# Kernel optimization log

Hardware: AMD Instinct MI355X
Metric: run time of the kernel (lower is better)

## Reference

```python
import jax, jax.numpy as jnp
import numpy as np

NO = 16          # config['Max_Object']
NT = 8           # config['Max_Time']
FEAT = 512       # config['feat_dims']
VIS_IN = 2048
TGT = 24


def setup_inputs() -> dict:
    key = jax.random.key(0)
    ks = jax.random.split(key, 10)
    b = 16
    N = NT * 2 * NO  # 256
    s = lambda k, *sh: jax.random.normal(k, sh, dtype=jnp.float32) * 0.02
    return {
        "src": jax.random.normal(ks[0], (b, 1, 1, N, VIS_IN), dtype=jnp.float32),
        "tgt_rel": jax.random.randint(ks[1], (b * NT * NO * NO,), 0, TGT, dtype=jnp.int64),
        "w1": s(ks[2], VIS_IN, FEAT), "b1": jnp.zeros((FEAT,), jnp.float32),
        "w2": s(ks[3], FEAT, FEAT),   "b2": jnp.zeros((FEAT,), jnp.float32),
        "wf": s(ks[4], FEAT, FEAT),   "bf": jnp.zeros((FEAT,), jnp.float32),
        "wr": s(ks[5], 2 * FEAT, TGT), "br": jnp.zeros((TGT,), jnp.float32),
    }


def reference(src, tgt_rel, w1, b1, w2, b2, wf, bf, wr, br):
    b = src.shape[0]
    BT = b * NT
    # src[:, 0, 0, :, :] -> (b, N, D) -> (b*NT, 2*NO, D); take visual part [:2048]
    x = src[:, 0, 0, :, :].reshape(BT, 2 * NO, -1)[:, :, :VIS_IN]
    # fc_vis: MLP 2048 -> FEAT -> FEAT
    h = jnp.maximum(x @ w1 + b1, 0.0) @ w2 + b2          # (BT, 2NO, FEAT)
    node_feats = h @ wf + bf                             # fc_fusion
    # vectorized replacement of the NOxNO python double loop:
    # edge[:, i*NO + (j-NO), :] = cat(node[:, i], node[:, j])  for i<NO<=j
    subj = jnp.broadcast_to(node_feats[:, :NO, None, :], (BT, NO, NO, FEAT))
    obj = jnp.broadcast_to(node_feats[:, None, NO:, :], (BT, NO, NO, FEAT))
    edge_feats = jnp.concatenate([subj, obj], axis=-1).reshape(BT, NO * NO, 2 * FEAT)
    out = (edge_feats @ wr + br).reshape(-1, TGT)        # fc_rel
    tgt = tgt_rel.reshape(-1)
    w_cls = jnp.asarray([1.0] + [100.0] * (TGT - 1), dtype=out.dtype)
    logp = jax.nn.log_softmax(out, axis=-1)
    nll = -jnp.take_along_axis(logp, tgt[:, None], axis=1)[:, 0]
    ww = w_cls[tgt]
    loss = jnp.sum(ww * nll) / jnp.sum(ww)  # torch weighted cross_entropy (mean)
    return out, tgt, loss
```

## Files before the change

### kernel.cpp

```cpp
#include <hip/hip_runtime.h>
#include <cstddef>
#include <cstdint>

#define NOBJ   16
#define FEAT   512
#define VIS    2048
#define NTGT   24
#define MROWS  4096
#define EROWS  32768

typedef __attribute__((ext_vector_type(8))) short short8;
typedef __attribute__((ext_vector_type(4))) float f32x4;

__device__ __forceinline__ float bf2f(unsigned short u) {
    union { unsigned int i; float f; } v; v.i = ((unsigned int)u) << 16; return v.f;
}
__device__ __forceinline__ unsigned short f2bf(float f) {
    union { float f; unsigned int i; } v; v.f = f;
    const unsigned int x = v.i;
    return (unsigned short)((x + 0x7fffu + ((x >> 16) & 1u)) >> 16);
}
__device__ __forceinline__ short8 pack8(const float4 a, const float4 b) {
    short8 r;
    r[0] = (short)f2bf(a.x); r[1] = (short)f2bf(a.y);
    r[2] = (short)f2bf(a.z); r[3] = (short)f2bf(a.w);
    r[4] = (short)f2bf(b.x); r[5] = (short)f2bf(b.y);
    r[6] = (short)f2bf(b.z); r[7] = (short)f2bf(b.w);
    return r;
}

__global__ void zero_kernel(float* __restrict__ p, int n) {
    const int i = blockIdx.x * 256 + threadIdx.x;
    if (i < n) p[i] = 0.f;
}

__global__ __launch_bounds__(256)
void wtrans(const float* __restrict__ w1, unsigned short* __restrict__ w1t) {
    __shared__ float tile[32][33];
    const int k0 = blockIdx.x * 32;
    const int n0 = blockIdx.y * 32;
    const int tx = threadIdx.x & 31, ty = threadIdx.x >> 5;
    #pragma unroll
    for (int r = 0; r < 32; r += 8)
        tile[ty + r][tx] = w1[(size_t)(k0 + ty + r) * FEAT + n0 + tx];
    __syncthreads();
    #pragma unroll
    for (int r = 0; r < 32; r += 8)
        w1t[(size_t)(n0 + ty + r) * VIS + k0 + tx] = f2bf(tile[tx][ty + r]);
}

__global__ __launch_bounds__(256)
void wchain1(const float* __restrict__ wf, const float* __restrict__ bfv,
             const float* __restrict__ wr, float* __restrict__ t1) {
    const int c    = threadIdx.x;
    const int krow = blockIdx.x * 8 + threadIdx.y;
    const int h    = blockIdx.z;
    const int j0   = blockIdx.y * 128;
    if (krow > 512) return;
    const float* rowp = (krow < 512) ? (wf + (size_t)krow * FEAT) : bfv;
    const int ce = (c < NTGT) ? c : NTGT - 1;
    const float* wrp = wr + ((size_t)h * FEAT + j0) * NTGT + ce;
    float s = 0.f;
    #pragma unroll 8
    for (int j = 0; j < 128; ++j)
        s = fmaf(rowp[j0 + j], wrp[(size_t)j * NTGT], s);
    if (c < NTGT) atomicAdd(&t1[((size_t)h * 513 + krow) * 32 + c], s);
}

__global__ __launch_bounds__(256)
void wchain2(const float* __restrict__ w2, const float* __restrict__ b2,
             const float* __restrict__ t1, float* __restrict__ wAB) {
    const int c  = threadIdx.x;
    const int r  = blockIdx.x * 8 + threadIdx.y;
    const int h  = blockIdx.z;
    const int k0 = blockIdx.y * 128;
    if (r > 512) return;
    const float* rowp = (r < 512) ? (w2 + (size_t)r * FEAT) : b2;
    const int ce = (c < NTGT) ? c : NTGT - 1;
    const float* tp = t1 + ((size_t)h * 513 + k0) * 32 + ce;
    float s = 0.f;
    #pragma unroll 8
    for (int k = 0; k < 128; ++k)
        s = fmaf(rowp[k0 + k], tp[(size_t)k * 32], s);
    if (r == 512 && blockIdx.y == 0)
        s += t1[((size_t)h * 513 + 512) * 32 + ce];
    if (c < NTGT) atomicAdd(&wAB[((size_t)h * 513 + r) * 32 + c], s);
}

__global__ __launch_bounds__(256)
void gemm1(const float* __restrict__ src, const unsigned short* __restrict__ w1t,
           const float* __restrict__ b1, unsigned short* __restrict__ h) {
    __shared__ __align__(16) unsigned short As[2][128 * 64];
    __shared__ __align__(16) unsigned short Bs[2][64 * 64];

    const int bid = blockIdx.x;
    const int xcd = bid & 7;
    const int k8  = bid >> 3;
    const int xb  = k8 & 7;
    const int yb  = (xcd << 2) | (k8 >> 3);
    const int m0 = yb * 128;
    const int n0 = xb * 64;

    const int tid  = threadIdx.x;
    const int lane = tid & 63;
    const int wid  = tid >> 6;
    const int wr = wid >> 1, wc = wid & 1;

    f32x4  acc[4][2] = {};
    float4 areg[4][2];
    short8 breg[2];

    #pragma unroll
    for (int q = 0; q < 4; ++q) {
        const int s = q * 256 + tid, row = s >> 3, c = s & 7, cd = c ^ (row & 7);
        const float* gp = src + (size_t)(m0 + row) * VIS + (cd << 3);
        areg[q][0] = *reinterpret_cast<const float4*>(gp);
        areg[q][1] = *reinterpret_cast<const float4*>(gp + 4);
    }
    #pragma unroll
    for (int q = 0; q < 2; ++q) {
        const int s = q * 256 + tid, n = s >> 3, c = s & 7, cd = c ^ (n & 7);
        breg[q] = *reinterpret_cast<const short8*>(w1t + (size_t)(n0 + n) * VIS + (cd << 3));
    }
    #pragma unroll
    for (int q = 0; q < 4; ++q) {
        const int s = q * 256 + tid, row = s >> 3, c = s & 7;
        *reinterpret_cast<short8*>(&As[0][(row << 6) + (c << 3)]) = pack8(areg[q][0], areg[q][1]);
    }
    #pragma unroll
    for (int q = 0; q < 2; ++q) {
        const int s = q * 256 + tid, n = s >> 3, c = s & 7;
        *reinterpret_cast<short8*>(&Bs[0][(n << 6) + (c << 3)]) = breg[q];
    }
    __syncthreads();

    int cur = 0;
    for (int t = 0; t < VIS / 64; ++t) {
        const int kn = (t + 1) * 64;
        if (t + 1 < VIS / 64) {
            #pragma unroll
            for (int q = 0; q < 4; ++q) {
                const int s = q * 256 + tid, row = s >> 3, c = s & 7, cd = c ^ (row & 7);
                const float* gp = src + (size_t)(m0 + row) * VIS + kn + (cd << 3);
                areg[q][0] = *reinterpret_cast<const float4*>(gp);
                areg[q][1] = *reinterpret_cast<const float4*>(gp + 4);
            }
            #pragma unroll
            for (int q = 0; q < 2; ++q) {
                const int s = q * 256 + tid, n = s >> 3, c = s & 7, cd = c ^ (n & 7);
                breg[q] = *reinterpret_cast<const short8*>(w1t + (size_t)(n0 + n) * VIS + kn + (cd << 3));
            }
        }
        #pragma unroll
        for (int k2 = 0; k2 < 2; ++k2) {
            short8 af[4], bfr[2];
            #pragma unroll
            for (int fr = 0; fr < 4; ++fr) {
                const int row = wr * 64 + fr * 16 + (lane & 15);
                const int cw  = ((k2 << 2) + (lane >> 4)) ^ (row & 7);
                af[fr] = *reinterpret_cast<const short8*>(&As[cur][(row << 6) + (cw << 3)]);
            }
            #pragma unroll
            for (int fc = 0; fc < 2; ++fc) {
                const int n  = wc * 32 + fc * 16 + (lane & 15);
                const int cw = ((k2 << 2) + (lane >> 4)) ^ (n & 7);
                bfr[fc] = *reinterpret_cast<const short8*>(&Bs[cur][(n << 6) + (cw << 3)]);
            }
            #pragma unroll
            for (int fr = 0; fr < 4; ++fr)
                #pragma unroll
                for (int fc = 0; fc < 2; ++fc)
                    acc[fr][fc] = __builtin_amdgcn_mfma_f32_16x16x32_bf16(
                        af[fr], bfr[fc], acc[fr][fc], 0, 0, 0);
        }
        if (t + 1 < VIS / 64) {
            const int nxt = cur ^ 1;
            #pragma unroll
            for (int q = 0; q < 4; ++q) {
                const int s = q * 256 + tid, row = s >> 3, c = s & 7;
                *reinterpret_cast<short8*>(&As[nxt][(row << 6) + (c << 3)]) =
                    pack8(areg[q][0], areg[q][1]);
            }
            #pragma unroll
            for (int q = 0; q < 2; ++q) {
                const int s = q * 256 + tid, n = s >> 3, c = s & 7;
                *reinterpret_cast<short8*>(&Bs[nxt][(n << 6) + (c << 3)]) = breg[q];
            }
        }
        __syncthreads();
        cur ^= 1;
    }

    #pragma unroll
    for (int fc = 0; fc < 2; ++fc) {
        const int n = n0 + wc * 32 + fc * 16 + (lane & 15);
        const float bias = b1[n];
        #pragma unroll
        for (int fr = 0; fr < 4; ++fr) {
            const int mb = m0 + wr * 64 + fr * 16 + ((lane >> 4) << 2);
            #pragma unroll
            for (int r = 0; r < 4; ++r) {
                const float v = fmaxf(acc[fr][fc][r] + bias, 0.f);
                h[(size_t)(mb + r) * FEAT + n] = f2bf(v);
            }
        }
    }
}

__global__ __launch_bounds__(192)
void proj(const unsigned short* __restrict__ h, const float* __restrict__ wAB,
          float* __restrict__ Ap, float* __restrict__ Bp) {
    __shared__ float rows[8][FEAT];
    const int g0 = blockIdx.x * 8;
    const int hh = (g0 >> 4) & 1;
    const int tid = threadIdx.x;
    for (int s = tid; s < 512; s += 192) {
        const int row = s >> 6, c8 = (s & 63) << 3;
        short8 v = *reinterpret_cast<const short8*>(h + (size_t)(g0 + row) * FEAT + c8);
        #pragma unroll
        for (int e = 0; e < 8; ++e)
            rows[row][c8 + e] = bf2f((unsigned short)v[e]);
    }
    __syncthreads();
    const int c = tid % NTGT, rr = tid / NTGT;
    const float* wp = wAB + (size_t)hh * 513 * 32 + c;
    float s = 0.f;
    #pragma unroll 8
    for (int k = 0; k < FEAT; ++k)
        s = fmaf(rows[rr][k], wp[(size_t)k * 32], s);
    s += wp[(size_t)512 * 32];
    const int g = g0 + rr, bt = g >> 5, i = g & 15;
    float* dst = (g & 16) ? Bp : Ap;
    dst[((size_t)bt * NOBJ + i) * NTGT + c] = s;
}

__global__ __launch_bounds__(256)
void out_loss_kernel(const float* __restrict__ Ap, const float* __restrict__ Bp,
                     const float* __restrict__ br, const int* __restrict__ tgt,
                     float* __restrict__ out, float* __restrict__ out_tgt,
                     float* __restrict__ acc) {
    const int r   = blockIdx.x * 256 + threadIdx.x;
    const int bt  = r >> 8;
    const int rem = r & 255;
    const int i   = rem >> 4;
    const int j   = rem & 15;
    const float4* ap4 = reinterpret_cast<const float4*>(Ap + ((size_t)bt * NOBJ + i) * NTGT);
    const float4* bp4 = reinterpret_cast<const float4*>(Bp + ((size_t)bt * NOBJ + j) * NTGT);
    const int tg = tgt[r];

    float vals[NTGT];
    float mx = -1e30f, vtg = 0.f;
    #pragma unroll
    for (int q = 0; q < 6; ++q) {
        const float4 a = ap4[q], b = bp4[q];
        vals[q * 4 + 0] = a.x + b.x + br[q * 4 + 0];
        vals[q * 4 + 1] = a.y + b.y + br[q * 4 + 1];
        vals[q * 4 + 2] = a.z + b.z + br[q * 4 + 2];
        vals[q * 4 + 3] = a.w + b.w + br[q * 4 + 3];
    }
    #pragma unroll
    for (int t = 0; t < NTGT; ++t) {
        mx = fmaxf(mx, vals[t]);
        if (t == tg) vtg = vals[t];
    }
    float se = 0.f;
    #pragma unroll
    for (int t = 0; t < NTGT; ++t) se += expf(vals[t] - mx);
    const float lse = mx + logf(se);

    float4* o4 = reinterpret_cast<float4*>(out + (size_t)r * NTGT);
    #pragma unroll
    for (int q = 0; q < 6; ++q)
        o4[q] = make_float4(vals[q * 4], vals[q * 4 + 1], vals[q * 4 + 2], vals[q * 4 + 3]);
    out_tgt[r] = (float)tg;

    const float wcl = (tg == 0) ? 1.f : 100.f;
    float p1 = wcl * (lse - vtg);
    float p2 = wcl;
    #pragma unroll
    for (int off = 32; off > 0; off >>= 1) {
        p1 += __shfl_down(p1, off);
        p2 += __shfl_down(p2, off);
    }
    __shared__ float s1[4], s2[4];
    const int lane = threadIdx.x & 63;
    const int wid  = threadIdx.x >> 6;
    if (lane == 0) { s1[wid] = p1; s2[wid] = p2; }
    __syncthreads();
    if (threadIdx.x == 0) {
        atomicAdd(&acc[0], s1[0] + s1[1] + s1[2] + s1[3]);
        atomicAdd(&acc[1], s2[0] + s2[1] + s2[2] + s2[3]);
    }
}

__global__ void final_loss(const float* __restrict__ acc, float* __restrict__ loss) {
    loss[0] = acc[0] / acc[1];
}

extern "C" void kernel_launch(void* const* d_in, const int* in_sizes, int n_in,
                              void* d_out, int out_size, void* d_ws, size_t ws_size,
                              hipStream_t stream) {
    const float* src = (const float*)d_in[0];
    const int*   tgt = (const int*)d_in[1];
    const float* w1  = (const float*)d_in[2];
    const float* b1  = (const float*)d_in[3];
    const float* w2  = (const float*)d_in[4];
    const float* b2  = (const float*)d_in[5];
    const float* wf  = (const float*)d_in[6];
    const float* bfv = (const float*)d_in[7];
    const float* wr  = (const float*)d_in[8];
    const float* br  = (const float*)d_in[9];

    float* ws = (float*)d_ws;
    unsigned short* w1t = (unsigned short*)(ws);
    unsigned short* h   = (unsigned short*)(ws + 524288);
    float* t1  = ws + 1572864;
    float* wAB = ws + 1605696;
    float* acc = ws + 1638528;
    float* Ap  = ws + 1638532;
    float* Bp  = ws + 1687684;

    float* out_logits = (float*)d_out;
    float* out_tgt    = out_logits + (size_t)EROWS * NTGT;
    float* out_lossp  = out_tgt + EROWS;

    zero_kernel<<<257, 256, 0, stream>>>(t1, 65666);
    wtrans<<<dim3(64, 16), 256, 0, stream>>>(w1, w1t);
    wchain1<<<dim3(65, 4, 2), dim3(32, 8), 0, stream>>>(wf, bfv, wr, t1);
    wchain2<<<dim3(65, 4, 2), dim3(32, 8), 0, stream>>>(w2, b2, t1, wAB);
    gemm1<<<256, 256, 0, stream>>>(src, w1t, b1, h);
    proj<<<512, 192, 0, stream>>>(h, wAB, Ap, Bp);
    out_loss_kernel<<<EROWS / 256, 256, 0, stream>>>(Ap, Bp, br, tgt,
                                                     out_logits, out_tgt, acc);
    final_loss<<<1, 1, 0, stream>>>(acc, out_lossp);
}
```

Baseline: 172.3 us.

## Restructure weight chain, projection, gemm tiling and loss reduction pipeline

```diff
diff --git a/kernel.cpp b/kernel.cpp
--- a/kernel.cpp
+++ b/kernel.cpp
@@ -12,9 +12,6 @@
 typedef __attribute__((ext_vector_type(8))) short short8;
 typedef __attribute__((ext_vector_type(4))) float f32x4;
 
-__device__ __forceinline__ float bf2f(unsigned short u) {
-    union { unsigned int i; float f; } v; v.i = ((unsigned int)u) << 16; return v.f;
-}
 __device__ __forceinline__ unsigned short f2bf(float f) {
     union { float f; unsigned int i; } v; v.f = f;
     const unsigned int x = v.i;
@@ -29,11 +26,6 @@
     return r;
 }
 
-__global__ void zero_kernel(float* __restrict__ p, int n) {
-    const int i = blockIdx.x * 256 + threadIdx.x;
-    if (i < n) p[i] = 0.f;
-}
-
 __global__ __launch_bounds__(256)
 void wtrans(const float* __restrict__ w1, unsigned short* __restrict__ w1t) {
     __shared__ float tile[32][33];
@@ -52,63 +44,72 @@
 __global__ __launch_bounds__(256)
 void wchain1(const float* __restrict__ wf, const float* __restrict__ bfv,
              const float* __restrict__ wr, float* __restrict__ t1) {
+    __shared__ float wrs[FEAT * NTGT];
+    const int h = blockIdx.y;
+    const float* wrh = wr + (size_t)h * FEAT * NTGT;
+    for (int idx = threadIdx.y * 32 + threadIdx.x; idx < FEAT * NTGT; idx += 256)
+        wrs[idx] = wrh[idx];
+    __syncthreads();
     const int c    = threadIdx.x;
     const int krow = blockIdx.x * 8 + threadIdx.y;
-    const int h    = blockIdx.z;
-    const int j0   = blockIdx.y * 128;
     if (krow > 512) return;
     const float* rowp = (krow < 512) ? (wf + (size_t)krow * FEAT) : bfv;
     const int ce = (c < NTGT) ? c : NTGT - 1;
-    const float* wrp = wr + ((size_t)h * FEAT + j0) * NTGT + ce;
     float s = 0.f;
     #pragma unroll 8
-    for (int j = 0; j < 128; ++j)
-        s = fmaf(rowp[j0 + j], wrp[(size_t)j * NTGT], s);
-    if (c < NTGT) atomicAdd(&t1[((size_t)h * 513 + krow) * 32 + c], s);
+    for (int j = 0; j < FEAT; ++j)
+        s = fmaf(rowp[j], wrs[j * NTGT + ce], s);
+    if (c < NTGT) t1[((size_t)h * 513 + krow) * 32 + c] = s;
 }
 
 __global__ __launch_bounds__(256)
 void wchain2(const float* __restrict__ w2, const float* __restrict__ b2,
-             const float* __restrict__ t1, float* __restrict__ wAB) {
-    const int c  = threadIdx.x;
-    const int r  = blockIdx.x * 8 + threadIdx.y;
-    const int h  = blockIdx.z;
-    const int k0 = blockIdx.y * 128;
+             const float* __restrict__ t1, unsigned short* __restrict__ wABt,
+             float* __restrict__ biasAB) {
+    __shared__ float t1s[FEAT * NTGT];
+    const int h = blockIdx.y;
+    for (int idx = threadIdx.y * 32 + threadIdx.x; idx < FEAT * NTGT; idx += 256) {
+        const int row = idx / NTGT, col = idx - row * NTGT;
+        t1s[idx] = t1[((size_t)h * 513 + row) * 32 + col];
+    }
+    __syncthreads();
+    const int c = threadIdx.x;
+    const int r = blockIdx.x * 8 + threadIdx.y;
     if (r > 512) return;
     const float* rowp = (r < 512) ? (w2 + (size_t)r * FEAT) : b2;
     const int ce = (c < NTGT) ? c : NTGT - 1;
-    const float* tp = t1 + ((size_t)h * 513 + k0) * 32 + ce;
     float s = 0.f;
     #pragma unroll 8
-    for (int k = 0; k < 128; ++k)
-        s = fmaf(rowp[k0 + k], tp[(size_t)k * 32], s);
-    if (r == 512 && blockIdx.y == 0)
-        s += t1[((size_t)h * 513 + 512) * 32 + ce];
-    if (c < NTGT) atomicAdd(&wAB[((size_t)h * 513 + r) * 32 + c], s);
+    for (int k = 0; k < FEAT; ++k)
+        s = fmaf(rowp[k], t1s[k * NTGT + ce], s);
+    if (c < NTGT) {
+        const int q = h * NTGT + c;
+        if (r < 512) wABt[(size_t)q * FEAT + r] = f2bf(s);
+        else         biasAB[q] = s + t1[((size_t)h * 513 + 512) * 32 + c];
+    }
 }
 
 __global__ __launch_bounds__(256)
 void gemm1(const float* __restrict__ src, const unsigned short* __restrict__ w1t,
            const float* __restrict__ b1, unsigned short* __restrict__ h) {
     __shared__ __align__(16) unsigned short As[2][128 * 64];
-    __shared__ __align__(16) unsigned short Bs[2][64 * 64];
+    __shared__ __align__(16) unsigned short Bs[2][32 * 64];
 
     const int bid = blockIdx.x;
     const int xcd = bid & 7;
     const int k8  = bid >> 3;
-    const int xb  = k8 & 7;
-    const int yb  = (xcd << 2) | (k8 >> 3);
+    const int xb  = k8 & 15;
+    const int yb  = (xcd << 2) | (k8 >> 4);
     const int m0 = yb * 128;
-    const int n0 = xb * 64;
+    const int n0 = xb * 32;
 
     const int tid  = threadIdx.x;
     const int lane = tid & 63;
     const int wid  = tid >> 6;
-    const int wr = wid >> 1, wc = wid & 1;
-
-    f32x4  acc[4][2] = {};
+
+    f32x4  acc[2][2] = {};
     float4 areg[4][2];
-    short8 breg[2];
+    short8 breg;
 
     #pragma unroll
     for (int q = 0; q < 4; ++q) {
@@ -117,20 +118,18 @@
         areg[q][0] = *reinterpret_cast<const float4*>(gp);
         areg[q][1] = *reinterpret_cast<const float4*>(gp + 4);
     }
-    #pragma unroll
-    for (int q = 0; q < 2; ++q) {
-        const int s = q * 256 + tid, n = s >> 3, c = s & 7, cd = c ^ (n & 7);
-        breg[q] = *reinterpret_cast<const short8*>(w1t + (size_t)(n0 + n) * VIS + (cd << 3));
+    {
+        const int n = tid >> 3, c = tid & 7, cd = c ^ (n & 7);
+        breg = *reinterpret_cast<const short8*>(w1t + (size_t)(n0 + n) * VIS + (cd << 3));
     }
     #pragma unroll
     for (int q = 0; q < 4; ++q) {
         const int s = q * 256 + tid, row = s >> 3, c = s & 7;
         *reinterpret_cast<short8*>(&As[0][(row << 6) + (c << 3)]) = pack8(areg[q][0], areg[q][1]);
     }
-    #pragma unroll
-    for (int q = 0; q < 2; ++q) {
-        const int s = q * 256 + tid, n = s >> 3, c = s & 7;
-        *reinterpret_cast<short8*>(&Bs[0][(n << 6) + (c << 3)]) = breg[q];
+    {
+        const int n = tid >> 3, c = tid & 7;
+        *reinterpret_cast<short8*>(&Bs[0][(n << 6) + (c << 3)]) = breg;
     }
     __syncthreads();
 
@@ -145,29 +144,26 @@
                 areg[q][0] = *reinterpret_cast<const float4*>(gp);
                 areg[q][1] = *reinterpret_cast<const float4*>(gp + 4);
             }
-            #pragma unroll
-            for (int q = 0; q < 2; ++q) {
-                const int s = q * 256 + tid, n = s >> 3, c = s & 7, cd = c ^ (n & 7);
-                breg[q] = *reinterpret_cast<const short8*>(w1t + (size_t)(n0 + n) * VIS + kn + (cd << 3));
-            }
+            const int n = tid >> 3, c = tid & 7, cd = c ^ (n & 7);
+            breg = *reinterpret_cast<const short8*>(w1t + (size_t)(n0 + n) * VIS + kn + (cd << 3));
         }
         #pragma unroll
         for (int k2 = 0; k2 < 2; ++k2) {
-            short8 af[4], bfr[2];
-            #pragma unroll
-            for (int fr = 0; fr < 4; ++fr) {
-                const int row = wr * 64 + fr * 16 + (lane & 15);
+            short8 af[2], bfr[2];
+            #pragma unroll
+            for (int fr = 0; fr < 2; ++fr) {
+                const int row = wid * 32 + fr * 16 + (lane & 15);
                 const int cw  = ((k2 << 2) + (lane >> 4)) ^ (row & 7);
                 af[fr] = *reinterpret_cast<const short8*>(&As[cur][(row << 6) + (cw << 3)]);
             }
             #pragma unroll
             for (int fc = 0; fc < 2; ++fc) {
-                const int n  = wc * 32 + fc * 16 + (lane & 15);
+                const int n  = fc * 16 + (lane & 15);
                 const int cw = ((k2 << 2) + (lane >> 4)) ^ (n & 7);
                 bfr[fc] = *reinterpret_cast<const short8*>(&Bs[cur][(n << 6) + (cw << 3)]);
             }
             #pragma unroll
-            for (int fr = 0; fr < 4; ++fr)
+            for (int fr = 0; fr < 2; ++fr)
                 #pragma unroll
                 for (int fc = 0; fc < 2; ++fc)
                     acc[fr][fc] = __builtin_amdgcn_mfma_f32_16x16x32_bf16(
@@ -181,11 +177,8 @@
                 *reinterpret_cast<short8*>(&As[nxt][(row << 6) + (c << 3)]) =
                     pack8(areg[q][0], areg[q][1]);
             }
-            #pragma unroll
-            for (int q = 0; q < 2; ++q) {
-                const int s = q * 256 + tid, n = s >> 3, c = s & 7;
-                *reinterpret_cast<short8*>(&Bs[nxt][(n << 6) + (c << 3)]) = breg[q];
-            }
+            const int n = tid >> 3, c = tid & 7;
+            *reinterpret_cast<short8*>(&Bs[nxt][(n << 6) + (c << 3)]) = breg;
         }
         __syncthreads();
         cur ^= 1;
@@ -193,11 +186,11 @@
 
     #pragma unroll
     for (int fc = 0; fc < 2; ++fc) {
-        const int n = n0 + wc * 32 + fc * 16 + (lane & 15);
+        const int n = n0 + fc * 16 + (lane & 15);
         const float bias = b1[n];
         #pragma unroll
-        for (int fr = 0; fr < 4; ++fr) {
-            const int mb = m0 + wr * 64 + fr * 16 + ((lane >> 4) << 2);
+        for (int fr = 0; fr < 2; ++fr) {
+            const int mb = m0 + wid * 32 + fr * 16 + ((lane >> 4) << 2);
             #pragma unroll
             for (int r = 0; r < 4; ++r) {
                 const float v = fmaxf(acc[fr][fc][r] + bias, 0.f);
@@ -207,61 +200,92 @@
     }
 }
 
-__global__ __launch_bounds__(192)
-void proj(const unsigned short* __restrict__ h, const float* __restrict__ wAB,
-          float* __restrict__ Ap, float* __restrict__ Bp) {
-    __shared__ float rows[8][FEAT];
-    const int g0 = blockIdx.x * 8;
-    const int hh = (g0 >> 4) & 1;
+__global__ __launch_bounds__(256)
+void projG(const unsigned short* __restrict__ h, const unsigned short* __restrict__ wABt,
+           const float* __restrict__ biasAB, float* __restrict__ P) {
+    __shared__ __align__(16) unsigned short Bs[64 * 512];
+    __shared__ __align__(16) unsigned short As[32 * 64];
+    const int tid  = threadIdx.x;
+    const int lane = tid & 63;
+    const int wid  = tid >> 6;
+    const int m0   = blockIdx.x * 32;
+
+    #pragma unroll
+    for (int q = 0; q < 16; ++q) {
+        const int e = q * 256 + tid;
+        const int n = e >> 6, cc = e & 63, cd = cc ^ (n & 7);
+        *reinterpret_cast<short8*>(&Bs[(n << 9) + (cc << 3)]) =
+            *reinterpret_cast<const short8*>(wABt + ((size_t)n << 9) + (cd << 3));
+    }
+    __syncthreads();
+
+    f32x4 acc[2] = {};
+    for (int t = 0; t < FEAT / 64; ++t) {
+        const int kt = t * 64;
+        {
+            const int row = tid >> 3, c = tid & 7, cd = c ^ (row & 7);
+            *reinterpret_cast<short8*>(&As[(row << 6) + (c << 3)]) =
+                *reinterpret_cast<const short8*>(h + (size_t)(m0 + row) * FEAT + kt + (cd << 3));
+        }
+        __syncthreads();
+        #pragma unroll
+        for (int k2 = 0; k2 < 2; ++k2) {
+            short8 af[2], bfr;
+            #pragma unroll
+            for (int fr = 0; fr < 2; ++fr) {
+                const int row = fr * 16 + (lane & 15);
+                const int cw  = ((k2 << 2) + (lane >> 4)) ^ (row & 7);
+                af[fr] = *reinterpret_cast<const short8*>(&As[(row << 6) + (cw << 3)]);
+            }
+            {
+                const int n     = wid * 16 + (lane & 15);
+                const int chunk = t * 8 + k2 * 4 + (lane >> 4);
+                const int cw    = chunk ^ (n & 7);
+                bfr = *reinterpret_cast<const short8*>(&Bs[(n << 9) + (cw << 3)]);
+            }
+            #pragma unroll
+            for (int fr = 0; fr < 2; ++fr)
+                acc[fr] = __builtin_amdgcn_mfma_f32_16x16x32_bf16(af[fr], bfr, acc[fr], 0, 0, 0);
+        }
+        __syncthreads();
+    }
+
+    const int n = wid * 16 + (lane & 15);
+    const float bias = biasAB[n];
+    #pragma unroll
+    for (int fr = 0; fr < 2; ++fr) {
+        const int rb = fr * 16 + ((lane >> 4) << 2);
+        #pragma unroll
+        for (int r = 0; r < 4; ++r)
+            P[(size_t)(m0 + rb + r) * 64 + n] = acc[fr][r] + bias;
+    }
+}
+
+__global__ __launch_bounds__(256)
+void out_loss_kernel(const float* __restrict__ P, const float* __restrict__ br,
+                     const int* __restrict__ tgt, float* __restrict__ out,
+                     float* __restrict__ out_tgt, float* __restrict__ partials) {
+    __shared__ float sm[32][49];
+    const int bt  = blockIdx.x;
     const int tid = threadIdx.x;
-    for (int s = tid; s < 512; s += 192) {
-        const int row = s >> 6, c8 = (s & 63) << 3;
-        short8 v = *reinterpret_cast<const short8*>(h + (size_t)(g0 + row) * FEAT + c8);
-        #pragma unroll
-        for (int e = 0; e < 8; ++e)
-            rows[row][c8 + e] = bf2f((unsigned short)v[e]);
-    }
-    __syncthreads();
-    const int c = tid % NTGT, rr = tid / NTGT;
-    const float* wp = wAB + (size_t)hh * 513 * 32 + c;
-    float s = 0.f;
-    #pragma unroll 8
-    for (int k = 0; k < FEAT; ++k)
-        s = fmaf(rows[rr][k], wp[(size_t)k * 32], s);
-    s += wp[(size_t)512 * 32];
-    const int g = g0 + rr, bt = g >> 5, i = g & 15;
-    float* dst = (g & 16) ? Bp : Ap;
-    dst[((size_t)bt * NOBJ + i) * NTGT + c] = s;
-}
-
-__global__ __launch_bounds__(256)
-void out_loss_kernel(const float* __restrict__ Ap, const float* __restrict__ Bp,
-                     const float* __restrict__ br, const int* __restrict__ tgt,
-                     float* __restrict__ out, float* __restrict__ out_tgt,
-                     float* __restrict__ acc) {
-    const int r   = blockIdx.x * 256 + threadIdx.x;
-    const int bt  = r >> 8;
-    const int rem = r & 255;
-    const int i   = rem >> 4;
-    const int j   = rem & 15;
-    const float4* ap4 = reinterpret_cast<const float4*>(Ap + ((size_t)bt * NOBJ + i) * NTGT);
-    const float4* bp4 = reinterpret_cast<const float4*>(Bp + ((size_t)bt * NOBJ + j) * NTGT);
+    for (int idx = tid; idx < 32 * 48; idx += 256) {
+        const int row = idx / 48, col = idx - row * 48;
+        sm[row][col] = P[(size_t)(bt * 32 + row) * 64 + col];
+    }
+    __syncthreads();
+
+    const int r  = bt * 256 + tid;
+    const int i  = tid >> 4, j = tid & 15;
     const int tg = tgt[r];
 
     float vals[NTGT];
     float mx = -1e30f, vtg = 0.f;
     #pragma unroll
-    for (int q = 0; q < 6; ++q) {
-        const float4 a = ap4[q], b = bp4[q];
-        vals[q * 4 + 0] = a.x + b.x + br[q * 4 + 0];
-        vals[q * 4 + 1] = a.y + b.y + br[q * 4 + 1];
-        vals[q * 4 + 2] = a.z + b.z + br[q * 4 + 2];
-        vals[q * 4 + 3] = a.w + b.w + br[q * 4 + 3];
-    }
-    #pragma unroll
     for (int t = 0; t < NTGT; ++t) {
-        mx = fmaxf(mx, vals[t]);
-        if (t == tg) vtg = vals[t];
+        const float v = sm[i][t] + sm[16 + j][24 + t] + br[t];
+        vals[t] = v;
+        mx = fmaxf(mx, v);
+        if (t == tg) vtg = v;
     }
     float se = 0.f;
     #pragma unroll
@@ -283,18 +307,25 @@
         p2 += __shfl_down(p2, off);
     }
     __shared__ float s1[4], s2[4];
-    const int lane = threadIdx.x & 63;
-    const int wid  = threadIdx.x >> 6;
-    if (lane == 0) { s1[wid] = p1; s2[wid] = p2; }
-    __syncthreads();
-    if (threadIdx.x == 0) {
-        atomicAdd(&acc[0], s1[0] + s1[1] + s1[2] + s1[3]);
-        atomicAdd(&acc[1], s2[0] + s2[1] + s2[2] + s2[3]);
-    }
-}
-
-__global__ void final_loss(const float* __restrict__ acc, float* __restrict__ loss) {
-    loss[0] = acc[0] / acc[1];
+    const int lane = tid & 63, wv = tid >> 6;
+    if (lane == 0) { s1[wv] = p1; s2[wv] = p2; }
+    __syncthreads();
+    if (tid == 0) {
+        partials[bt]       = s1[0] + s1[1] + s1[2] + s1[3];
+        partials[128 + bt] = s2[0] + s2[1] + s2[2] + s2[3];
+    }
+}
+
+__global__ void final_loss(const float* __restrict__ partials, float* __restrict__ loss) {
+    const int t = threadIdx.x;
+    float a = partials[t] + partials[t + 64];
+    float b = partials[128 + t] + partials[192 + t];
+    #pragma unroll
+    for (int off = 32; off > 0; off >>= 1) {
+        a += __shfl_down(a, off);
+        b += __shfl_down(b, off);
+    }
+    if (t == 0) loss[0] = a / b;
 }
 
 extern "C" void kernel_launch(void* const* d_in, const int* in_sizes, int n_in,
@@ -312,25 +343,23 @@
     const float* br  = (const float*)d_in[9];
 
     float* ws = (float*)d_ws;
-    unsigned short* w1t = (unsigned short*)(ws);
-    unsigned short* h   = (unsigned short*)(ws + 524288);
-    float* t1  = ws + 1572864;
-    float* wAB = ws + 1605696;
-    float* acc = ws + 1638528;
-    float* Ap  = ws + 1638532;
-    float* Bp  = ws + 1687684;
+    unsigned short* w1t  = (unsigned short*)(ws);
+    unsigned short* h    = (unsigned short*)(ws + 524288);
+    float*          t1   = ws + 1572864;
+    unsigned short* wABt = (unsigned short*)(ws + 1605696);
+    float*          biasAB = ws + 1622080;
+    float*          P    = ws + 1622144;
+    float*          parts = ws + 1884288;
 
     float* out_logits = (float*)d_out;
     float* out_tgt    = out_logits + (size_t)EROWS * NTGT;
     float* out_lossp  = out_tgt + EROWS;
 
-    zero_kernel<<<257, 256, 0, stream>>>(t1, 65666);
     wtrans<<<dim3(64, 16), 256, 0, stream>>>(w1, w1t);
-    wchain1<<<dim3(65, 4, 2), dim3(32, 8), 0, stream>>>(wf, bfv, wr, t1);
-    wchain2<<<dim3(65, 4, 2), dim3(32, 8), 0, stream>>>(w2, b2, t1, wAB);
-    gemm1<<<256, 256, 0, stream>>>(src, w1t, b1, h);
-    proj<<<512, 192, 0, stream>>>(h, wAB, Ap, Bp);
-    out_loss_kernel<<<EROWS / 256, 256, 0, stream>>>(Ap, Bp, br, tgt,
-                                                     out_logits, out_tgt, acc);
-    final_loss<<<1, 1, 0, stream>>>(acc, out_lossp);
-}
+    wchain1<<<dim3(65, 2), dim3(32, 8), 0, stream>>>(wf, bfv, wr, t1);
+    wchain2<<<dim3(65, 2), dim3(32, 8), 0, stream>>>(w2, b2, t1, wABt, biasAB);
+    gemm1<<<512, 256, 0, stream>>>(src, w1t, b1, h);
+    projG<<<128, 256, 0, stream>>>(h, wABt, biasAB, P);
+    out_loss_kernel<<<128, 256, 0, stream>>>(P, br, tgt, out_logits, out_tgt, parts);
+    final_loss<<<1, 64, 0, stream>>>(parts, out_lossp);
+}
```

Result: faster. 163.7 us (-5.0%).
